# Performance work log

Hardware: AMD Instinct MI355X
Metric: run time of the kernel (lower is better)

## Reference

```python
import jax, jax.numpy as jnp
import numpy as np

TEMPERATURE = 0.07
BASE_TEMPERATURE = 0.07


def setup_inputs() -> dict:
    key = jax.random.key(0)
    k1, k2 = jax.random.split(key)
    feat1 = jax.random.normal(k1, (4096, 128), dtype=jnp.float32)
    feat2 = jax.random.normal(k2, (4096, 128), dtype=jnp.float32)
    return {"feat1": feat1, "feat2": feat2}


def reference(feat1, feat2):
    # world_size = 1 -> gather is identity; N = per-gpu batch size
    N = feat1.shape[0]
    two_n = 2 * N
    features = jnp.concatenate([feat1, feat2], axis=0)          # [2N, C]
    # F.normalize(dim=1)
    norm = jnp.linalg.norm(features, axis=1, keepdims=True)
    features = features / jnp.maximum(norm, 1e-12)
    logits = jnp.matmul(features, features.T) / TEMPERATURE      # [2N, 2N]
    logits = logits - jax.lax.stop_gradient(
        jnp.max(logits, axis=1, keepdims=True))
    # neg_mask = ~eye: sum of exp over off-diagonal entries per row
    exp_sum = jnp.sum(jnp.exp(logits), axis=1) - jnp.exp(jnp.diagonal(logits))
    # pos_mask: row i pairs with column (i + N) mod 2N
    idx = jnp.arange(two_n)
    pos = logits[idx, (idx + N) % two_n]                          # [2N]
    log_prob = pos - jnp.log(exp_sum)
    loss = -(TEMPERATURE / BASE_TEMPERATURE) * jnp.mean(log_prob)
    return loss
```

## Files before the change

### kernel.cpp

```cpp
#include <hip/hip_runtime.h>

typedef unsigned short u16;
typedef __attribute__((ext_vector_type(8))) short short8;
typedef __attribute__((ext_vector_type(4))) float f32x4;

#define INVT 14.285714285714286f
#define EXP2C 20.609640474436812f

__device__ __forceinline__ u16 f2bf(float f) {
  union { float f; unsigned u; } v; v.f = f;
  unsigned u = v.u;
  u += 0x7fffu + ((u >> 16) & 1u);
  return (u16)(u >> 16);
}
__device__ __forceinline__ float bf2f(u16 h) {
  union { unsigned u; float f; } v; v.u = ((unsigned)h) << 16;
  return v.f;
}

__device__ __forceinline__ float fast_exp2(float x) {
#if __has_builtin(__builtin_amdgcn_exp2f)
  return __builtin_amdgcn_exp2f(x);
#else
  return exp2f(x);
#endif
}

__global__ void norm_kernel(const float* __restrict__ f1, const float* __restrict__ f2,
                            u16* __restrict__ F, float* __restrict__ dvec,
                            float* __restrict__ pos, float* __restrict__ E, int N) {
  int i = blockIdx.x;
  int l = threadIdx.x;
  if (l < 2) E[2 * i + l] = 0.0f;
  const float* a = f1 + (size_t)i * 128;
  const float* b = f2 + (size_t)i * 128;
  float a0 = a[l], a1 = a[l + 64];
  float b0 = b[l], b1 = b[l + 64];
  float sa = a0 * a0 + a1 * a1;
  float sb = b0 * b0 + b1 * b1;
#pragma unroll
  for (int o = 32; o; o >>= 1) { sa += __shfl_xor(sa, o); sb += __shfl_xor(sb, o); }
  float ia = 1.0f / fmaxf(sqrtf(sa), 1e-12f);
  float ib = 1.0f / fmaxf(sqrtf(sb), 1e-12f);
  u16 ba0 = f2bf(a0 * ia), ba1 = f2bf(a1 * ia);
  u16 bb0 = f2bf(b0 * ib), bb1 = f2bf(b1 * ib);
  u16* Fa = F + (size_t)i * 128;
  u16* Fb = F + (size_t)(i + N) * 128;
  Fa[l] = ba0; Fa[l + 64] = ba1;
  Fb[l] = bb0; Fb[l + 64] = bb1;
  float fa0 = bf2f(ba0), fa1 = bf2f(ba1);
  float fb0 = bf2f(bb0), fb1 = bf2f(bb1);
  float s1 = fa0 * fa0 + fa1 * fa1;
  float s2 = fb0 * fb0 + fb1 * fb1;
  float cr = fa0 * fb0 + fa1 * fb1;
#pragma unroll
  for (int o = 32; o; o >>= 1) {
    s1 += __shfl_xor(s1, o); s2 += __shfl_xor(s2, o); cr += __shfl_xor(cr, o);
  }
  if (l == 0) {
    dvec[i]     = fast_exp2(fmaf(s1, EXP2C, -EXP2C));
    dvec[i + N] = fast_exp2(fmaf(s2, EXP2C, -EXP2C));
    pos[i] = cr;
    pos[i + N] = cr;
  }
}

__device__ __forceinline__ void glds16(const u16* g, u16* l) {
  __builtin_amdgcn_global_load_lds((const __attribute__((address_space(1))) void*)g,
                                   (__attribute__((address_space(3))) void*)l,
                                   16, 0, 0);
}

template <int CTRL>
__device__ __forceinline__ float ror_add(float x) {
  int r = __builtin_amdgcn_update_dpp(0, __float_as_int(x), CTRL, 0xF, 0xF, false);
  return x + __int_as_float(r);
}

__global__ __launch_bounds__(512, 4) void gemm_exp_kernel(const u16* __restrict__ F,
                                                          float* __restrict__ E) {
  __shared__ __align__(16) u16 At[2][128][64];
  __shared__ __align__(16) u16 Bt[2][128][64];
  __shared__ float colsum[128];
  __shared__ float rowsum[128];
  const int tid = threadIdx.x;
  const int wave = tid >> 6, lane = tid & 63;
  int p = blockIdx.x;
  int r = (int)((sqrtf(8.0f * (float)p + 1.0f) - 1.0f) * 0.5f);
  while ((r + 1) * (r + 2) / 2 <= p) ++r;
  while (r * (r + 1) / 2 > p) --r;
  const int bj = r, bi = p - r * (r + 1) / 2;
  const u16* __restrict__ Ab = F + (size_t)bi * (128 * 128);
  const u16* __restrict__ Bb = F + (size_t)bj * (128 * 128);
  if (tid < 128) { colsum[tid] = 0.0f; rowsum[tid] = 0.0f; }

  const int lrow = lane >> 3, lcol = lane & 7;
#pragma unroll
  for (int h = 0; h < 2; ++h)
#pragma unroll
    for (int t = 0; t < 2; ++t) {
      const int row = wave * 16 + t * 8 + lrow;
      const size_t gsrc = (size_t)(row * 16 + h * 8 + (lcol ^ (row & 7))) * 8;
      u16* da = (u16*)At + h * 8192 + (wave * 2 + t) * 512;
      u16* db = (u16*)Bt + h * 8192 + (wave * 2 + t) * 512;
      glds16(Ab + gsrc, da);
      glds16(Bb + gsrc, db);
    }

  const int wr = wave >> 1, wc = wave & 1;
  const int q = lane >> 4, m = lane & 15;
  f32x4 acc[2][4];
#pragma unroll
  for (int fr = 0; fr < 2; ++fr)
#pragma unroll
    for (int cf = 0; cf < 4; ++cf) acc[fr][cf] = (f32x4)(0.0f);

  auto kstep = [&](int ks) {
    const int h = ks >> 1;
    const int c = (ks & 1) * 4 + q;
    const u16* Ah = (const u16*)At + h * 8192;
    const u16* Bh = (const u16*)Bt + h * 8192;
    short8 av[2], bv[4];
#pragma unroll
    for (int fr = 0; fr < 2; ++fr) {
      int rr = wr * 32 + fr * 16 + m;
      av[fr] = *(const short8*)&Ah[rr * 64 + ((c ^ (rr & 7)) * 8)];
    }
#pragma unroll
    for (int cf = 0; cf < 4; ++cf) {
      int rr = wc * 64 + cf * 16 + m;
      bv[cf] = *(const short8*)&Bh[rr * 64 + ((c ^ (rr & 7)) * 8)];
    }
#pragma unroll
    for (int fr = 0; fr < 2; ++fr)
#pragma unroll
      for (int cf = 0; cf < 4; ++cf)
        acc[fr][cf] = __builtin_amdgcn_mfma_f32_16x16x32_bf16(av[fr], bv[cf], acc[fr][cf], 0, 0, 0);
  };

  asm volatile("s_waitcnt vmcnt(4) lgkmcnt(0)\n\ts_barrier" ::: "memory");
  kstep(0);
  kstep(1);
  asm volatile("s_waitcnt vmcnt(0)\n\ts_barrier" ::: "memory");
  kstep(2);
  kstep(3);

  float cs[4] = {0.f, 0.f, 0.f, 0.f};
  float rs[8] = {0.f, 0.f, 0.f, 0.f, 0.f, 0.f, 0.f, 0.f};
#pragma unroll
  for (int cf = 0; cf < 4; ++cf)
#pragma unroll
    for (int fr = 0; fr < 2; ++fr)
#pragma unroll
      for (int rg = 0; rg < 4; ++rg) {
        float e = fast_exp2(fmaf(acc[fr][cf][rg], EXP2C, -EXP2C));
        cs[cf] += e;
        rs[fr * 4 + rg] += e;
      }
#pragma unroll
  for (int cf = 0; cf < 4; ++cf) {
    cs[cf] += __shfl_xor(cs[cf], 16);
    cs[cf] += __shfl_xor(cs[cf], 32);
    if (q == 0) atomicAdd(&colsum[wc * 64 + cf * 16 + m], cs[cf]);
  }
  if (bi != bj) {
#pragma unroll
    for (int i = 0; i < 8; ++i) {
      float v = rs[i];
      v = ror_add<0x121>(v);
      v = ror_add<0x122>(v);
      v = ror_add<0x124>(v);
      v = ror_add<0x128>(v);
      if (m == i) atomicAdd(&rowsum[wr * 32 + (i >> 2) * 16 + q * 4 + (i & 3)], v);
    }
  }
  __syncthreads();
  if (tid < 128) {
    atomicAdd(&E[bj * 128 + tid], colsum[tid]);
    if (bi != bj) atomicAdd(&E[bi * 128 + tid], rowsum[tid]);
  }
}

__global__ void finish_kernel(const float* __restrict__ E, const float* __restrict__ dvec,
                              const float* __restrict__ pos, float* __restrict__ out,
                              int TWO_N, float scale) {
  float t = 0.0f;
  for (int i = threadIdx.x; i < TWO_N; i += 1024)
    t += (pos[i] - 1.0f) * INVT - logf(E[i] - dvec[i]);
#pragma unroll
  for (int o = 32; o; o >>= 1) t += __shfl_xor(t, o);
  __shared__ float wsum[16];
  int wave = threadIdx.x >> 6, lane = threadIdx.x & 63;
  if (lane == 0) wsum[wave] = t;
  __syncthreads();
  if (threadIdx.x == 0) {
    float s = 0.0f;
#pragma unroll
    for (int k = 0; k < 16; ++k) s += wsum[k];
    out[0] = s * scale;
  }
}

extern "C" void kernel_launch(void* const* d_in, const int* in_sizes, int n_in,
                              void* d_out, int out_size, void* d_ws, size_t ws_size,
                              hipStream_t stream) {
  const float* f1 = (const float*)d_in[0];
  const float* f2 = (const float*)d_in[1];
  const int N = in_sizes[0] / 128;
  const int TWO_N = 2 * N;
  const int NB = TWO_N / 128;
  const int NTILES = NB * (NB + 1) / 2;

  char* ws = (char*)d_ws;
  u16*   F    = (u16*)ws;
  float* dvec = (float*)(ws + (size_t)TWO_N * 128 * 2);
  float* pos  = dvec + TWO_N;
  float* E    = pos + TWO_N;

  norm_kernel<<<N, 64, 0, stream>>>(f1, f2, F, dvec, pos, E, N);
  gemm_exp_kernel<<<NTILES, 512, 0, stream>>>(F, E);
  finish_kernel<<<1, 1024, 0, stream>>>(E, dvec, pos, (float*)d_out, TWO_N,
                                        -1.0f / (float)TWO_N);
}
```

Before: 83.95 us.

## Enlarge symmetric GEMM tiles to 256x256 and pack four rows per norm block

The fused GEMM+exp kernel now computes 256x256 output tiles per block instead of 128x128. That quarters the tile count and halves the operand loads per output element, and the epilogue, atomics and launch bounds are rescaled to match. The normalization kernel now handles four rows per 256-thread block with float2 loads and packed 32-bit bf16 stores, cutting per-block launch overhead. Costs: 128 accumulator floats per thread raise register pressure and lower occupancy, there are far fewer blocks (136) to spread across the CUs, and diagonal tiles waste more work.

```diff
diff --git a/kernel.cpp b/kernel.cpp
--- a/kernel.cpp
+++ b/kernel.cpp
@@ -26,28 +26,26 @@
 #endif
 }
 
-__global__ void norm_kernel(const float* __restrict__ f1, const float* __restrict__ f2,
-                            u16* __restrict__ F, float* __restrict__ dvec,
-                            float* __restrict__ pos, float* __restrict__ E, int N) {
-  int i = blockIdx.x;
-  int l = threadIdx.x;
-  if (l < 2) E[2 * i + l] = 0.0f;
-  const float* a = f1 + (size_t)i * 128;
-  const float* b = f2 + (size_t)i * 128;
-  float a0 = a[l], a1 = a[l + 64];
-  float b0 = b[l], b1 = b[l + 64];
-  float sa = a0 * a0 + a1 * a1;
-  float sb = b0 * b0 + b1 * b1;
+__global__ __launch_bounds__(256) void norm_kernel(const float* __restrict__ f1,
+                                                   const float* __restrict__ f2,
+                                                   u16* __restrict__ F, float* __restrict__ dvec,
+                                                   float* __restrict__ pos, float* __restrict__ E,
+                                                   int N) {
+  const int wave = threadIdx.x >> 6, l = threadIdx.x & 63;
+  const int i = blockIdx.x * 4 + wave;
+  if (threadIdx.x < 8) E[blockIdx.x * 8 + threadIdx.x] = 0.0f;
+  const float2 a = ((const float2*)(f1 + (size_t)i * 128))[l];
+  const float2 b = ((const float2*)(f2 + (size_t)i * 128))[l];
+  float sa = a.x * a.x + a.y * a.y;
+  float sb = b.x * b.x + b.y * b.y;
 #pragma unroll
   for (int o = 32; o; o >>= 1) { sa += __shfl_xor(sa, o); sb += __shfl_xor(sb, o); }
   float ia = 1.0f / fmaxf(sqrtf(sa), 1e-12f);
   float ib = 1.0f / fmaxf(sqrtf(sb), 1e-12f);
-  u16 ba0 = f2bf(a0 * ia), ba1 = f2bf(a1 * ia);
-  u16 bb0 = f2bf(b0 * ib), bb1 = f2bf(b1 * ib);
-  u16* Fa = F + (size_t)i * 128;
-  u16* Fb = F + (size_t)(i + N) * 128;
-  Fa[l] = ba0; Fa[l + 64] = ba1;
-  Fb[l] = bb0; Fb[l + 64] = bb1;
+  u16 ba0 = f2bf(a.x * ia), ba1 = f2bf(a.y * ia);
+  u16 bb0 = f2bf(b.x * ib), bb1 = f2bf(b.y * ib);
+  ((unsigned*)(F + (size_t)i * 128))[l]       = (unsigned)ba0 | ((unsigned)ba1 << 16);
+  ((unsigned*)(F + (size_t)(i + N) * 128))[l] = (unsigned)bb0 | ((unsigned)bb1 << 16);
   float fa0 = bf2f(ba0), fa1 = bf2f(ba1);
   float fb0 = bf2f(bb0), fb1 = bf2f(bb1);
   float s1 = fa0 * fa0 + fa1 * fa1;
@@ -77,80 +75,82 @@
   return x + __int_as_float(r);
 }
 
-__global__ __launch_bounds__(512, 4) void gemm_exp_kernel(const u16* __restrict__ F,
+__global__ __launch_bounds__(512, 2) void gemm_exp_kernel(const u16* __restrict__ F,
                                                           float* __restrict__ E) {
-  __shared__ __align__(16) u16 At[2][128][64];
-  __shared__ __align__(16) u16 Bt[2][128][64];
-  __shared__ float colsum[128];
-  __shared__ float rowsum[128];
+  __shared__ __align__(16) u16 At[2][256][64];
+  __shared__ __align__(16) u16 Bt[2][256][64];
+  __shared__ float colsum[256];
+  __shared__ float rowsum[256];
   const int tid = threadIdx.x;
   const int wave = tid >> 6, lane = tid & 63;
   int p = blockIdx.x;
   int r = (int)((sqrtf(8.0f * (float)p + 1.0f) - 1.0f) * 0.5f);
   while ((r + 1) * (r + 2) / 2 <= p) ++r;
   while (r * (r + 1) / 2 > p) --r;
-  const int bj = r, bi = p - r * (r + 1) / 2;
-  const u16* __restrict__ Ab = F + (size_t)bi * (128 * 128);
-  const u16* __restrict__ Bb = F + (size_t)bj * (128 * 128);
-  if (tid < 128) { colsum[tid] = 0.0f; rowsum[tid] = 0.0f; }
+  const int sj = r, si = p - r * (r + 1) / 2;
+  const u16* __restrict__ Ab = F + (size_t)si * (256 * 128);
+  const u16* __restrict__ Bb = F + (size_t)sj * (256 * 128);
+  if (tid < 256) { colsum[tid] = 0.0f; rowsum[tid] = 0.0f; }
 
   const int lrow = lane >> 3, lcol = lane & 7;
 #pragma unroll
   for (int h = 0; h < 2; ++h)
 #pragma unroll
-    for (int t = 0; t < 2; ++t) {
-      const int row = wave * 16 + t * 8 + lrow;
+    for (int t = 0; t < 4; ++t) {
+      const int row = (wave * 4 + t) * 8 + lrow;
       const size_t gsrc = (size_t)(row * 16 + h * 8 + (lcol ^ (row & 7))) * 8;
-      u16* da = (u16*)At + h * 8192 + (wave * 2 + t) * 512;
-      u16* db = (u16*)Bt + h * 8192 + (wave * 2 + t) * 512;
+      u16* da = (u16*)At + h * 16384 + (wave * 4 + t) * 512;
+      u16* db = (u16*)Bt + h * 16384 + (wave * 4 + t) * 512;
       glds16(Ab + gsrc, da);
       glds16(Bb + gsrc, db);
     }
 
   const int wr = wave >> 1, wc = wave & 1;
   const int q = lane >> 4, m = lane & 15;
-  f32x4 acc[2][4];
-#pragma unroll
-  for (int fr = 0; fr < 2; ++fr)
-#pragma unroll
-    for (int cf = 0; cf < 4; ++cf) acc[fr][cf] = (f32x4)(0.0f);
+  f32x4 acc[4][8];
+#pragma unroll
+  for (int fr = 0; fr < 4; ++fr)
+#pragma unroll
+    for (int cf = 0; cf < 8; ++cf) acc[fr][cf] = (f32x4)(0.0f);
 
   auto kstep = [&](int ks) {
     const int h = ks >> 1;
     const int c = (ks & 1) * 4 + q;
-    const u16* Ah = (const u16*)At + h * 8192;
-    const u16* Bh = (const u16*)Bt + h * 8192;
-    short8 av[2], bv[4];
-#pragma unroll
-    for (int fr = 0; fr < 2; ++fr) {
-      int rr = wr * 32 + fr * 16 + m;
+    const u16* Ah = (const u16*)At + h * 16384;
+    const u16* Bh = (const u16*)Bt + h * 16384;
+    short8 av[4], bv[8];
+#pragma unroll
+    for (int fr = 0; fr < 4; ++fr) {
+      int rr = wr * 64 + fr * 16 + m;
       av[fr] = *(const short8*)&Ah[rr * 64 + ((c ^ (rr & 7)) * 8)];
     }
 #pragma unroll
-    for (int cf = 0; cf < 4; ++cf) {
-      int rr = wc * 64 + cf * 16 + m;
+    for (int cf = 0; cf < 8; ++cf) {
+      int rr = wc * 128 + cf * 16 + m;
       bv[cf] = *(const short8*)&Bh[rr * 64 + ((c ^ (rr & 7)) * 8)];
     }
 #pragma unroll
-    for (int fr = 0; fr < 2; ++fr)
-#pragma unroll
-      for (int cf = 0; cf < 4; ++cf)
+    for (int fr = 0; fr < 4; ++fr)
+#pragma unroll
+      for (int cf = 0; cf < 8; ++cf)
         acc[fr][cf] = __builtin_amdgcn_mfma_f32_16x16x32_bf16(av[fr], bv[cf], acc[fr][cf], 0, 0, 0);
   };
 
-  asm volatile("s_waitcnt vmcnt(4) lgkmcnt(0)\n\ts_barrier" ::: "memory");
+  asm volatile("s_waitcnt vmcnt(8) lgkmcnt(0)\n\ts_barrier" ::: "memory");
   kstep(0);
   kstep(1);
   asm volatile("s_waitcnt vmcnt(0)\n\ts_barrier" ::: "memory");
   kstep(2);
   kstep(3);
 
-  float cs[4] = {0.f, 0.f, 0.f, 0.f};
-  float rs[8] = {0.f, 0.f, 0.f, 0.f, 0.f, 0.f, 0.f, 0.f};
-#pragma unroll
-  for (int cf = 0; cf < 4; ++cf)
-#pragma unroll
-    for (int fr = 0; fr < 2; ++fr)
+  float cs[8] = {0.f, 0.f, 0.f, 0.f, 0.f, 0.f, 0.f, 0.f};
+  float rs[16];
+#pragma unroll
+  for (int i = 0; i < 16; ++i) rs[i] = 0.f;
+#pragma unroll
+  for (int cf = 0; cf < 8; ++cf)
+#pragma unroll
+    for (int fr = 0; fr < 4; ++fr)
 #pragma unroll
       for (int rg = 0; rg < 4; ++rg) {
         float e = fast_exp2(fmaf(acc[fr][cf][rg], EXP2C, -EXP2C));
@@ -158,26 +158,26 @@
         rs[fr * 4 + rg] += e;
       }
 #pragma unroll
-  for (int cf = 0; cf < 4; ++cf) {
+  for (int cf = 0; cf < 8; ++cf) {
     cs[cf] += __shfl_xor(cs[cf], 16);
     cs[cf] += __shfl_xor(cs[cf], 32);
-    if (q == 0) atomicAdd(&colsum[wc * 64 + cf * 16 + m], cs[cf]);
-  }
-  if (bi != bj) {
-#pragma unroll
-    for (int i = 0; i < 8; ++i) {
+    if (q == 0) atomicAdd(&colsum[wc * 128 + cf * 16 + m], cs[cf]);
+  }
+  if (si != sj) {
+#pragma unroll
+    for (int i = 0; i < 16; ++i) {
       float v = rs[i];
       v = ror_add<0x121>(v);
       v = ror_add<0x122>(v);
       v = ror_add<0x124>(v);
       v = ror_add<0x128>(v);
-      if (m == i) atomicAdd(&rowsum[wr * 32 + (i >> 2) * 16 + q * 4 + (i & 3)], v);
+      if (m == i) atomicAdd(&rowsum[wr * 64 + (i >> 2) * 16 + q * 4 + (i & 3)], v);
     }
   }
   __syncthreads();
-  if (tid < 128) {
-    atomicAdd(&E[bj * 128 + tid], colsum[tid]);
-    if (bi != bj) atomicAdd(&E[bi * 128 + tid], rowsum[tid]);
+  if (tid < 256) {
+    atomicAdd(&E[sj * 256 + tid], colsum[tid]);
+    if (si != sj) atomicAdd(&E[si * 256 + tid], rowsum[tid]);
   }
 }
 
@@ -208,8 +208,8 @@
   const float* f2 = (const float*)d_in[1];
   const int N = in_sizes[0] / 128;
   const int TWO_N = 2 * N;
-  const int NB = TWO_N / 128;
-  const int NTILES = NB * (NB + 1) / 2;
+  const int NB2 = TWO_N / 256;
+  const int NTILES = NB2 * (NB2 + 1) / 2;
 
   char* ws = (char*)d_ws;
   u16*   F    = (u16*)ws;
@@ -217,7 +217,7 @@
   float* pos  = dvec + TWO_N;
   float* E    = pos + TWO_N;
 
-  norm_kernel<<<N, 64, 0, stream>>>(f1, f2, F, dvec, pos, E, N);
+  norm_kernel<<<N / 4, 256, 0, stream>>>(f1, f2, F, dvec, pos, E, N);
   gemm_exp_kernel<<<NTILES, 512, 0, stream>>>(F, E);
   finish_kernel<<<1, 1024, 0, stream>>>(E, dvec, pos, (float*)d_out, TWO_N,
                                         -1.0f / (float)TWO_N);
```

Result: no change. 85.15 us (+1.4%).

## Fuse final reduction into GEMM via last-block counter and mask diagonal in-tile

Applied to the files above, without the earlier changes.

Removes the separate finish kernel by having the last GEMM block, detected with an atomic tile counter, compute the log-sum and write the loss. The diagonal exp term is excluded directly inside diagonal tiles instead of being subtracted via a precomputed dvec. The norm kernel packs four rows per 256-thread block and uses vectorized float2 loads and packed stores. This saves a kernel launch and some memory traffic but hardcodes the tile count to 2080 and adds serialized tail work in one block.

```diff
diff --git a/kernel.cpp b/kernel.cpp
--- a/kernel.cpp
+++ b/kernel.cpp
@@ -6,6 +6,7 @@
 
 #define INVT 14.285714285714286f
 #define EXP2C 20.609640474436812f
+#define NTILES_C 2080
 
 __device__ __forceinline__ u16 f2bf(float f) {
   union { float f; unsigned u; } v; v.f = f;
@@ -26,43 +27,33 @@
 #endif
 }
 
-__global__ void norm_kernel(const float* __restrict__ f1, const float* __restrict__ f2,
-                            u16* __restrict__ F, float* __restrict__ dvec,
-                            float* __restrict__ pos, float* __restrict__ E, int N) {
-  int i = blockIdx.x;
-  int l = threadIdx.x;
-  if (l < 2) E[2 * i + l] = 0.0f;
-  const float* a = f1 + (size_t)i * 128;
-  const float* b = f2 + (size_t)i * 128;
-  float a0 = a[l], a1 = a[l + 64];
-  float b0 = b[l], b1 = b[l + 64];
-  float sa = a0 * a0 + a1 * a1;
-  float sb = b0 * b0 + b1 * b1;
+__global__ __launch_bounds__(256) void norm_kernel(const float* __restrict__ f1,
+                                                   const float* __restrict__ f2,
+                                                   u16* __restrict__ F,
+                                                   float* __restrict__ pos, float* __restrict__ E,
+                                                   unsigned* __restrict__ cnt, int N) {
+  const int wave = threadIdx.x >> 6, l = threadIdx.x & 63;
+  const int i = blockIdx.x * 4 + wave;
+  if (threadIdx.x < 8) E[blockIdx.x * 8 + threadIdx.x] = 0.0f;
+  if (blockIdx.x == 0 && threadIdx.x == 8) *cnt = 0u;
+  const float2 a = ((const float2*)(f1 + (size_t)i * 128))[l];
+  const float2 b = ((const float2*)(f2 + (size_t)i * 128))[l];
+  float sa = a.x * a.x + a.y * a.y;
+  float sb = b.x * b.x + b.y * b.y;
 #pragma unroll
   for (int o = 32; o; o >>= 1) { sa += __shfl_xor(sa, o); sb += __shfl_xor(sb, o); }
   float ia = 1.0f / fmaxf(sqrtf(sa), 1e-12f);
   float ib = 1.0f / fmaxf(sqrtf(sb), 1e-12f);
-  u16 ba0 = f2bf(a0 * ia), ba1 = f2bf(a1 * ia);
-  u16 bb0 = f2bf(b0 * ib), bb1 = f2bf(b1 * ib);
-  u16* Fa = F + (size_t)i * 128;
-  u16* Fb = F + (size_t)(i + N) * 128;
-  Fa[l] = ba0; Fa[l + 64] = ba1;
-  Fb[l] = bb0; Fb[l + 64] = bb1;
+  u16 ba0 = f2bf(a.x * ia), ba1 = f2bf(a.y * ia);
+  u16 bb0 = f2bf(b.x * ib), bb1 = f2bf(b.y * ib);
+  ((unsigned*)(F + (size_t)i * 128))[l]       = (unsigned)ba0 | ((unsigned)ba1 << 16);
+  ((unsigned*)(F + (size_t)(i + N) * 128))[l] = (unsigned)bb0 | ((unsigned)bb1 << 16);
   float fa0 = bf2f(ba0), fa1 = bf2f(ba1);
   float fb0 = bf2f(bb0), fb1 = bf2f(bb1);
-  float s1 = fa0 * fa0 + fa1 * fa1;
-  float s2 = fb0 * fb0 + fb1 * fb1;
   float cr = fa0 * fb0 + fa1 * fb1;
 #pragma unroll
-  for (int o = 32; o; o >>= 1) {
-    s1 += __shfl_xor(s1, o); s2 += __shfl_xor(s2, o); cr += __shfl_xor(cr, o);
-  }
-  if (l == 0) {
-    dvec[i]     = fast_exp2(fmaf(s1, EXP2C, -EXP2C));
-    dvec[i + N] = fast_exp2(fmaf(s2, EXP2C, -EXP2C));
-    pos[i] = cr;
-    pos[i + N] = cr;
-  }
+  for (int o = 32; o; o >>= 1) cr += __shfl_xor(cr, o);
+  if (l == 0) { pos[i] = cr; pos[i + N] = cr; }
 }
 
 __device__ __forceinline__ void glds16(const u16* g, u16* l) {
@@ -78,11 +69,16 @@
 }
 
 __global__ __launch_bounds__(512, 4) void gemm_exp_kernel(const u16* __restrict__ F,
-                                                          float* __restrict__ E) {
+                                                          float* __restrict__ E,
+                                                          const float* __restrict__ pos,
+                                                          unsigned* __restrict__ cnt,
+                                                          float* __restrict__ out,
+                                                          float scale) {
   __shared__ __align__(16) u16 At[2][128][64];
   __shared__ __align__(16) u16 Bt[2][128][64];
   __shared__ float colsum[128];
   __shared__ float rowsum[128];
+  __shared__ int last_flag;
   const int tid = threadIdx.x;
   const int wave = tid >> 6, lane = tid & 63;
   int p = blockIdx.x;
@@ -147,16 +143,30 @@
 
   float cs[4] = {0.f, 0.f, 0.f, 0.f};
   float rs[8] = {0.f, 0.f, 0.f, 0.f, 0.f, 0.f, 0.f, 0.f};
-#pragma unroll
-  for (int cf = 0; cf < 4; ++cf)
-#pragma unroll
-    for (int fr = 0; fr < 2; ++fr)
-#pragma unroll
-      for (int rg = 0; rg < 4; ++rg) {
-        float e = fast_exp2(fmaf(acc[fr][cf][rg], EXP2C, -EXP2C));
-        cs[cf] += e;
-        rs[fr * 4 + rg] += e;
+  if (bi != bj) {
+#pragma unroll
+    for (int cf = 0; cf < 4; ++cf)
+#pragma unroll
+      for (int fr = 0; fr < 2; ++fr)
+#pragma unroll
+        for (int rg = 0; rg < 4; ++rg) {
+          float e = fast_exp2(fmaf(acc[fr][cf][rg], EXP2C, -EXP2C));
+          cs[cf] += e;
+          rs[fr * 4 + rg] += e;
+        }
+  } else {
+#pragma unroll
+    for (int cf = 0; cf < 4; ++cf)
+#pragma unroll
+      for (int fr = 0; fr < 2; ++fr) {
+        const bool fragdiag = (wr * 2 + fr) == (wc * 4 + cf);
+#pragma unroll
+        for (int rg = 0; rg < 4; ++rg) {
+          float e = fast_exp2(fmaf(acc[fr][cf][rg], EXP2C, -EXP2C));
+          if (!(fragdiag && (q * 4 + rg) == m)) cs[cf] += e;
+        }
       }
+  }
 #pragma unroll
   for (int cf = 0; cf < 4; ++cf) {
     cs[cf] += __shfl_xor(cs[cf], 16);
@@ -179,25 +189,29 @@
     atomicAdd(&E[bj * 128 + tid], colsum[tid]);
     if (bi != bj) atomicAdd(&E[bi * 128 + tid], rowsum[tid]);
   }
-}
-
-__global__ void finish_kernel(const float* __restrict__ E, const float* __restrict__ dvec,
-                              const float* __restrict__ pos, float* __restrict__ out,
-                              int TWO_N, float scale) {
-  float t = 0.0f;
-  for (int i = threadIdx.x; i < TWO_N; i += 1024)
-    t += (pos[i] - 1.0f) * INVT - logf(E[i] - dvec[i]);
-#pragma unroll
-  for (int o = 32; o; o >>= 1) t += __shfl_xor(t, o);
-  __shared__ float wsum[16];
-  int wave = threadIdx.x >> 6, lane = threadIdx.x & 63;
-  if (lane == 0) wsum[wave] = t;
+  __threadfence();
   __syncthreads();
-  if (threadIdx.x == 0) {
-    float s = 0.0f;
-#pragma unroll
-    for (int k = 0; k < 16; ++k) s += wsum[k];
-    out[0] = s * scale;
+  if (tid == 0) last_flag = (atomicAdd(cnt, 1u) == (unsigned)(NTILES_C - 1)) ? 1 : 0;
+  __syncthreads();
+  if (last_flag) {
+    __threadfence();
+    float t = 0.0f;
+#pragma unroll
+    for (int k = 0; k < 16; ++k) {
+      int i = tid + k * 512;
+      float e = atomicAdd(&E[i], 0.0f);
+      t += (pos[i] - 1.0f) * INVT - logf(e);
+    }
+#pragma unroll
+    for (int o = 32; o; o >>= 1) t += __shfl_xor(t, o);
+    if (lane == 0) colsum[wave] = t;
+    __syncthreads();
+    if (tid == 0) {
+      float s = 0.0f;
+#pragma unroll
+      for (int k = 0; k < 8; ++k) s += colsum[k];
+      out[0] = s * scale;
+    }
   }
 }
 
@@ -212,13 +226,12 @@
   const int NTILES = NB * (NB + 1) / 2;
 
   char* ws = (char*)d_ws;
-  u16*   F    = (u16*)ws;
-  float* dvec = (float*)(ws + (size_t)TWO_N * 128 * 2);
-  float* pos  = dvec + TWO_N;
-  float* E    = pos + TWO_N;
-
-  norm_kernel<<<N, 64, 0, stream>>>(f1, f2, F, dvec, pos, E, N);
-  gemm_exp_kernel<<<NTILES, 512, 0, stream>>>(F, E);
-  finish_kernel<<<1, 1024, 0, stream>>>(E, dvec, pos, (float*)d_out, TWO_N,
-                                        -1.0f / (float)TWO_N);
-}
+  u16*      F   = (u16*)ws;
+  float*    pos = (float*)(ws + (size_t)TWO_N * 128 * 2);
+  float*    E   = pos + TWO_N;
+  unsigned* cnt = (unsigned*)(E + TWO_N);
+
+  norm_kernel<<<N / 4, 256, 0, stream>>>(f1, f2, F, pos, E, cnt, N);
+  gemm_exp_kernel<<<NTILES, 512, 0, stream>>>(F, E, pos, cnt, (float*)d_out,
+                                              -1.0f / (float)TWO_N);
+}
```

Result: slower. 328.1 us (+290.8%).
